# Performance work log

Measured on AMD Instinct MI355X. Metric: run time of the kernel, lower is better.

## Reference

```python
import jax, jax.numpy as jnp
import numpy as np

S0 = 100.0
V0 = 0.04
RATE = 0.025
MC = 50000          # MC_samples; 2*MC antithetic paths
N_STEPS = 180       # == int(x[:,0].max()), pinned in setup_inputs for static shapes
WIDTH = 64
N_OPTS = 32
H = 1.0 / 360.0     # timegrid step: (maxT/360)/maxT


def setup_inputs():
    key = jax.random.key(0)
    ks = jax.random.split(key, 8)
    mat = jax.random.randint(ks[0], (N_OPTS,), 30, N_STEPS + 1).astype(jnp.float32)
    mat = mat.at[0].set(float(N_STEPS))  # pin max maturity -> static n_steps
    strikes = 80.0 + 40.0 * jax.random.uniform(ks[1], (N_OPTS,), dtype=jnp.float32)
    x = jnp.stack([mat, strikes], axis=1)  # [n_opts, 2]: (maturity_days, strike)
    z = jax.random.normal(ks[2], (MC, N_STEPS), dtype=jnp.float32)
    z1 = jax.random.normal(ks[3], (MC, N_STEPS), dtype=jnp.float32)
    # 4 stacked tiny MLPs: order = [driftS, diffusionS, driftV, diffusionV]
    W1 = 0.1 * jax.random.normal(ks[4], (4, WIDTH, 4), dtype=jnp.float32)
    b1 = jnp.zeros((4, WIDTH), jnp.float32)
    W2 = 0.1 * jax.random.normal(ks[5], (4, WIDTH, WIDTH), dtype=jnp.float32)
    b2 = jnp.zeros((4, WIDTH), jnp.float32)
    Wo = 0.05 * jax.random.normal(ks[6], (4, 1, WIDTH), dtype=jnp.float32)
    bo = jnp.zeros((4, 1), jnp.float32)
    return dict(x=x, z=z, z1=z1, W1=W1, b1=b1, W2=W2, b2=b2, Wo=Wo, bo=bo)


def _mlp4(inp, W1, b1, W2, b2, Wo, bo):
    # Evaluate the 4 tiny MLPs on the shared input [M,4] in one batched pass.
    h1 = jax.nn.relu(jnp.einsum('nwd,md->nmw', W1, inp) + b1[:, None, :])
    h2 = jax.nn.relu(jnp.einsum('nvw,nmw->nmv', W2, h1) + b2[:, None, :])
    out = jnp.einsum('now,nmw->nmo', Wo, h2) + bo[:, None, :]
    return out[..., 0]  # [4, M]


def _forward(x, z, z1, W1, b1, W2, b2, Wo, bo, remat=False):
    M = 2 * MC
    h = jnp.float32(H)
    sqh = jnp.sqrt(h)
    # correlated second Brownian: z1 <- -0.5*z + sqrt(0.75)*z1, then antithetic
    z1c = -0.5 * z + np.float32(np.sqrt(0.75)) * z1
    zf = jnp.concatenate([z, -z], axis=0)        # [M, T]
    z1f = jnp.concatenate([z1c, -z1c], axis=0)   # [M, T]
    tgrid = jnp.arange(N_STEPS, dtype=jnp.float32) * h  # t_{i-1}
    rate_col = jnp.full((M,), RATE, jnp.float32)

    def step(carry, xs):
        S, V = carry
        zc, z1cc, tc = xs
        dW = sqh * zc
        dW1 = sqh * z1cc
        inp = jnp.stack([jnp.full((M,), tc), S, V, rate_col], axis=1)  # [M,4]
        o = _mlp4(inp, W1, b1, W2, b2, Wo, bo)  # [4, M]
        Sn = jnp.maximum(S + o[0] * h + o[1] * dW, 0.0)   # max(., 0) clamp
        Vn = jnp.maximum(V + o[2] * h + o[3] * dW1, 0.0)
        return (Sn, Vn), Sn

    if remat:
        step = jax.checkpoint(step)
    init = (jnp.full((M,), S0, jnp.float32), jnp.full((M,), V0, jnp.float32))
    _, Spath = jax.lax.scan(step, init, (zf.T, z1f.T, tgrid))  # Spath: [T, M]
    Sample_path = jnp.concatenate([jnp.full((1, M), S0, jnp.float32), Spath], axis=0)  # [T+1, M]

    # vectorized option pricing over all rows of x
    idx = x[:, 0].astype(jnp.int32)                  # maturity index into path
    ST = Sample_path[idx]                            # [n_opts, M]
    payoff = jnp.maximum(ST - x[:, 1][:, None], 0.0)
    price = payoff.mean(axis=1) * jnp.exp(-RATE * x[:, 0] / 360.0)
    return price.reshape(-1, 1)


def reference(x, z, z1, W1, b1, W2, b2, Wo, bo):
    return _forward(x, z, z1, W1, b1, W2, b2, Wo, bo, remat=False)
```

## Files before the change

kernel.cpp:

```cpp
#include <hip/hip_runtime.h>
#include <math.h>

#define MC      50000
#define MPATHS  100000
#define NSTEPS  180
#define NOPTS   32

typedef __attribute__((ext_vector_type(8))) short short8;
typedef __attribute__((ext_vector_type(4))) float float4v;
typedef _Float16 half2v __attribute__((ext_vector_type(2)));
typedef unsigned u32x32 __attribute__((ext_vector_type(32)));

static __device__ __forceinline__ unsigned bf16u(float x) {
    unsigned u = __float_as_uint(x);
    return (u + 0x7fffu + ((u >> 16) & 1u)) >> 16;
}
static __device__ __forceinline__ float bf16val(float x) {
    return __uint_as_float(bf16u(x) << 16);
}
static __device__ __forceinline__ unsigned pkh2(float a, float b) {
    half2v h; h.x = (_Float16)a; h.y = (_Float16)b;
    return __builtin_bit_cast(unsigned, h);
}
static __device__ __forceinline__ unsigned pkrtz(float a, float b) {
    auto h = __builtin_amdgcn_cvt_pkrtz(a, b);
    return __builtin_bit_cast(unsigned, h);
}
static __device__ __forceinline__ float fdot2(unsigned w, unsigned h, float c) {
    return __builtin_amdgcn_fdot2(__builtin_bit_cast(half2v, w),
                                  __builtin_bit_cast(half2v, h), c, false);
}
static __device__ __forceinline__ short8 fr4(unsigned a, unsigned b,
                                             unsigned c, unsigned d) {
    union { unsigned u[4]; short8 s; } t;
    t.u[0] = a; t.u[1] = b; t.u[2] = c; t.u[3] = d;
    return t.s;
}
static __device__ __forceinline__ float4v mfma16(short8 a, short8 b, float4v c) {
    return __builtin_amdgcn_mfma_f32_16x16x32_bf16(a, b, c, 0, 0, 0);
}


__global__ void probe_mn(int* tbl) {
    const int lane = threadIdx.x;
    for (int s = lane; s < 2048; s += 64) tbl[s] = 0;
    const float4v z4 = {0.f, 0.f, 0.f, 0.f};
    for (int L = 0; L < 64; ++L)
        for (int j = 0; j < 8; ++j) {
            unsigned au[4] = {0u, 0u, 0u, 0u};
            if (lane == L) au[j >> 1] = 0x3F80u << (16 * (j & 1));
            short8 a = fr4(au[0], au[1], au[2], au[3]);
            short8 b = fr4(0x3F803F80u, 0x3F803F80u, 0x3F803F80u, 0x3F803F80u);
            float4v d = mfma16(a, b, z4);
            if ((lane & 15) == 0) {
                #pragma unroll
                for (int r = 0; r < 4; ++r)
                    if (d[r] != 0.0f) tbl[L * 8 + j] = (lane >> 4) * 4 + r;
            }
        }
    for (int L = 0; L < 64; ++L)
        for (int j = 0; j < 8; ++j) {
            unsigned bu[4] = {0u, 0u, 0u, 0u};
            if (lane == L) bu[j >> 1] = 0x3F80u << (16 * (j & 1));
            short8 a = fr4(0x3F803F80u, 0x3F803F80u, 0x3F803F80u, 0x3F803F80u);
            short8 b = fr4(bu[0], bu[1], bu[2], bu[3]);
            float4v d = mfma16(a, b, z4);
            if ((lane >> 4) == 0 && d[0] != 0.0f) tbl[1024 + L * 8 + j] = (lane & 15);
        }
}

__global__ void probe_k(int* tbl) {
    const int lane = threadIdx.x;
    const int sA = blockIdx.x;
    const float4v z4 = {0.f, 0.f, 0.f, 0.f};
    unsigned au[4] = {0u, 0u, 0u, 0u};
    if (lane == (sA >> 3)) au[(sA & 7) >> 1] = 0x3F80u << (16 * (sA & 1));
    short8 a = fr4(au[0], au[1], au[2], au[3]);
    int kid = -1;
    for (int sB = 0; sB < 512; ++sB) {
        unsigned bu[4] = {0u, 0u, 0u, 0u};
        const int LB = sB >> 3, jB = sB & 7;
        if (lane == LB) bu[jB >> 1] = 0x3F80u << (16 * (jB & 1));
        short8 b = fr4(bu[0], bu[1], bu[2], bu[3]);
        float4v d = mfma16(a, b, z4);
        bool hit = (d[0] != 0.f) | (d[1] != 0.f) | (d[2] != 0.f) | (d[3] != 0.f);
        if (__any(hit)) {
            if (kid < 0) kid = sB;
            if (lane == 0) tbl[1536 + sB] = kid;
        }
    }
    if (lane == 0) tbl[512 + sA] = (kid < 0) ? 0 : kid;
}

__global__ void finalize_verify(int* tbl, int* flag) {
    __shared__ int cnt[32];
    __shared__ int minv[32];
    const int lane = threadIdx.x;
    if (lane < 32) { cnt[lane] = 0; minv[lane] = 0; }
    int rA[8], rB[8];
    #pragma unroll
    for (int j = 0; j < 8; ++j) {
        const int s = lane * 8 + j;
        const int kidA = tbl[512 + s], kidB = tbl[1536 + s];
        int ra = 0, rb = 0;
        for (int u = 0; u < 512; ++u) {
            const int canon = (tbl[1536 + u] == u);
            ra += canon & (u < kidA);
            rb += canon & (u < kidB);
        }
        rA[j] = ra & 31; rB[j] = rb & 31;
    }
    __syncthreads();
    #pragma unroll
    for (int j = 0; j < 8; ++j) {
        tbl[512 + lane * 8 + j]  = rA[j];
        tbl[1536 + lane * 8 + j] = rB[j];
    }
    unsigned au[4] = {0u, 0u, 0u, 0u}, bu[4] = {0u, 0u, 0u, 0u};
    #pragma unroll
    for (int j = 0; j < 8; ++j) {
        const int s = lane * 8 + j;
        const int m = tbl[s] & 15, ka = rA[j];
        const int n = tbl[1024 + s] & 15, kb = rB[j];
        const int fv = ((m * 7 + ka * 3) % 5) - 2;
        const int gv = ((kb * 5 + n * 11) % 7) - 3;
        au[j >> 1] |= bf16u((float)fv) << (16 * (j & 1));
        bu[j >> 1] |= bf16u((float)gv) << (16 * (j & 1));
    }
    const float4v z4 = {0.f, 0.f, 0.f, 0.f};
    float4v d = mfma16(fr4(au[0], au[1], au[2], au[3]),
                       fr4(bu[0], bu[1], bu[2], bu[3]), z4);
    const int col = lane & 15;
    bool ok = true;
    #pragma unroll
    for (int r = 0; r < 4; ++r) {
        const int row = (lane >> 4) * 4 + r;
        int ref = 0;
        for (int k = 0; k < 32; ++k)
            ref += (((row * 7 + k * 3) % 5) - 2) * (((k * 5 + col * 11) % 7) - 3);
        ok = ok && (d[r] == (float)ref);
    }
    bool okf = ok;
    #pragma unroll
    for (int j = 0; j < 8; ++j) {
        okf = okf && ((tbl[1024 + lane * 8 + j] & 15) == (lane & 15));
        const int ref = __shfl(rB[j], lane & 48, 64);
        okf = okf && (rB[j] == ref);
    }
    if ((lane & 15) == 0) {
        const int g = lane >> 4;
        #pragma unroll
        for (int j = 0; j < 8; ++j) {
            atomicAdd(&cnt[rB[j]], 1);
            minv[rB[j]] = 16 * ((j >> 2) & 1) + 4 * g + 2 * ((j >> 1) & 1) + (j & 1);
        }
    }
    __syncthreads();
    if (lane < 32) {
        okf = okf && (cnt[lane] == 1);
        tbl[2048 + lane] = minv[lane];
    }
    const bool allok = __all(okf);
    if (lane == 0) *flag = allok ? 1 : 0;
}

__global__ void build_frags(const float* __restrict__ W1, const float* __restrict__ b1,
                            const float* __restrict__ W2, const int* __restrict__ tbl,
                            uint4* __restrict__ w1f, uint4* __restrict__ w2f) {
    const int t = blockIdx.x * 256 + threadIdx.x;
    if (t >= 3072) return;
    const int lane = t & 63, frag = t >> 6;
    const float rateB = bf16val(0.025f);
    unsigned u[4] = {0u, 0u, 0u, 0u};
    if (frag < 16) {
        const int net = frag >> 2, mt = frag & 3;
        #pragma unroll
        for (int j = 0; j < 8; ++j) {
            const int s = lane * 8 + j;
            const int m = tbl[s] & 15, k = tbl[512 + s] & 31;
            unsigned bits = 0u;
            if (k < 12) {
                const int kk = (k < 6) ? k : k - 6;
                const int M = net * 64 + 16 * mt + m;
                float v;
                if (kk == 0)                 v = W1[M * 4 + 0];
                else if (kk == 1 || kk == 4) v = W1[M * 4 + 1];
                else if (kk == 2 || kk == 5) v = W1[M * 4 + 2];
                else                         v = W1[M * 4 + 3] + b1[M] / rateB;
                bits = (k < 6) ? bf16u(v) : bf16u(v - bf16val(v));
            }
            u[j >> 1] |= bits << (16 * (j & 1));
        }
        w1f[frag * 64 + lane] = make_uint4(u[0], u[1], u[2], u[3]);
    } else {
        const int f2 = frag - 16;
        const int net = f2 >> 3, mt = (f2 >> 1) & 3, kc = f2 & 1;
        #pragma unroll
        for (int j = 0; j < 8; ++j) {
            const int s = lane * 8 + j;
            const int m = tbl[s] & 15, k = tbl[512 + s] & 31;
            const float v = W2[(net * 64 + 16 * mt + m) * 64 + 32 * kc + tbl[2048 + k]];
            u[j >> 1] |= bf16u(v) << (16 * (j & 1));
        }
        w2f[f2 * 64 + lane] = make_uint4(u[0], u[1], u[2], u[3]);
    }
}

__global__ __launch_bounds__(256, 3)
void sde_mfma_w4(const float* __restrict__ x, const float* __restrict__ z,
                 const float* __restrict__ z1, const float* __restrict__ b2,
                 const float* __restrict__ Wo, const float* __restrict__ bo,
                 const int* __restrict__ tbl, const uint4* __restrict__ w1f,
                 const uint4* __restrict__ w2f, const int* __restrict__ flag,
                 float* __restrict__ acc)
{
    if (*flag != 1) return;
    __shared__ __align__(16) float wo_s[256];
    __shared__ __align__(16) float b2_s[256];
    __shared__ float dxch[2][4][64];
    __shared__ float ls_k[NOPTS];
    __shared__ int   maskTab[NSTEPS + 4];

    const int tid = threadIdx.x;
    const int wv = tid >> 6, lane = tid & 63;
    const int q = lane >> 4, c = lane & 15;

    for (int j = tid; j < 256; j += 256) { wo_s[j] = Wo[j]; b2_s[j] = b2[j]; }
    for (int j = tid; j < NSTEPS + 4; j += 256) maskTab[j] = 0;
    if (tid < NOPTS) ls_k[tid] = x[2 * tid + 1];
    __syncthreads();
    if (tid < NOPTS) atomicOr(&maskTab[(int)x[2 * tid]], 1 << tid);
    __syncthreads();

    const unsigned rate16 = bf16u(0.025f);
    unsigned selAB[4], dynM[4], cU[4], mT[4];
    {
        int rowj[8];
        #pragma unroll
        for (int j = 0; j < 8; ++j) {
            const int kb = tbl[1536 + lane * 8 + j] & 31;
            rowj[j] = (kb < 6) ? kb : ((kb < 12) ? kb - 6 : 6);
        }
        #pragma unroll
        for (int w = 0; w < 4; ++w) {
            unsigned s = 0, d = 0, cu = 0, mt_ = 0;
            #pragma unroll
            for (int h = 0; h < 2; ++h) {
                const int r = rowj[2 * w + h];
                unsigned hs = 0x0504u, hd = 0u, hcu = 0u, hmt = 0u;
                if      (r == 1) { hs = 0x0504u; hd = 0xFFFFu; }
                else if (r == 2) { hs = 0x0706u; hd = 0xFFFFu; }
                else if (r == 4) { hs = 0x0100u; hd = 0xFFFFu; }
                else if (r == 5) { hs = 0x0302u; hd = 0xFFFFu; }
                else if (r == 0) { hmt = 0xFFFFu; }
                else if (r == 3) { hcu = rate16; }
                s  |= hs  << (16 * h); d   |= hd  << (16 * h);
                cu |= hcu << (16 * h); mt_ |= hmt << (16 * h);
            }
            selAB[w] = s; dynM[w] = d; cU[w] = cu; mT[w] = mt_;
        }
    }

    const int p_ = blockIdx.x * 64 + lane;
    const float wgt = (p_ < MPATHS) ? 1.0f : 0.0f;
    int pc = (p_ < MPATHS) ? p_ : (MPATHS - 1);
    float sgn = 1.0f; int row_ = pc;
    if (pc >= MC) { sgn = -1.0f; row_ -= MC; }
    const float* __restrict__ zrow  = z  + (size_t)row_ * NSTEPS;
    const float* __restrict__ z1row = z1 + (size_t)row_ * NSTEPS;

    const float hh = 1.0f / 360.0f, sqh = sqrtf(hh);
    const float s75 = 0.86602540378443864676f;
    const float bon = bo[wv];

    uint4 a1f[4], a2f[8];
    #pragma unroll
    for (int mt = 0; mt < 4; ++mt) {
        a1f[mt]         = w1f[(wv * 4 + mt) * 64 + lane];
        a2f[2 * mt]     = w2f[((wv * 4 + mt) * 2 + 0) * 64 + lane];
        a2f[2 * mt + 1] = w2f[((wv * 4 + mt) * 2 + 1) * 64 + lane];
    }

    float S = 100.0f, V = 0.04f;

    #pragma unroll 1
    for (int i = 0; i < NSTEPS; ++i) {
        float mult;
        if      (wv == 1) mult = sqh * (sgn * zrow[i]);
        else if (wv == 3) mult = sqh * (sgn * (-0.5f * zrow[i] + s75 * z1row[i]));
        else              mult = hh;

        const float t = (float)i * hh;
        const unsigned tB = bf16u(t);
        const unsigned tB2 = tB | (tB << 16);
        unsigned UW[4];
        #pragma unroll
        for (int w = 0; w < 4; ++w) UW[w] = cU[w] | (mT[w] & tB2);

        const unsigned Shu = bf16u(S), Vhu = bf16u(V);
        const unsigned PA = Shu | (Vhu << 16);
        const float Sr = S - __uint_as_float(Shu << 16);
        const float Vr = V - __uint_as_float(Vhu << 16);
        const unsigned PB = __builtin_amdgcn_perm(__float_as_uint(Vr),
                                                  __float_as_uint(Sr), 0x07060302u);

        unsigned B1[4][4];
        #pragma unroll
        for (int nt = 0; nt < 4; ++nt) {
            const int a = (nt << 6) | (c << 2);
            const unsigned Ap = (unsigned)__builtin_amdgcn_ds_bpermute(a, (int)PA);
            const unsigned Bp = (unsigned)__builtin_amdgcn_ds_bpermute(a, (int)PB);
            #pragma unroll
            for (int w = 0; w < 4; ++w)
                B1[nt][w] = (__builtin_amdgcn_perm(Ap, Bp, selAB[w]) & dynM[w]) | UW[w];
        }

        float part[4] = {0.f, 0.f, 0.f, 0.f};
        const float4v z4 = {0.f, 0.f, 0.f, 0.f};
        #pragma unroll
        for (int nt = 0; nt < 4; ++nt) {
            unsigned pk0[4], pk1[4];
            #pragma unroll
            for (int mt = 0; mt < 4; ++mt) {
                float4v d = mfma16(fr4(a1f[mt].x, a1f[mt].y, a1f[mt].z, a1f[mt].w),
                                   fr4(B1[nt][0], B1[nt][1], B1[nt][2], B1[nt][3]), z4);
                const unsigned r0 = __float_as_uint(fmaxf(d[0], 0.f));
                const unsigned r1 = __float_as_uint(fmaxf(d[1], 0.f));
                const unsigned r2 = __float_as_uint(fmaxf(d[2], 0.f));
                const unsigned r3 = __float_as_uint(fmaxf(d[3], 0.f));
                pk0[mt] = __builtin_amdgcn_perm(r1, r0, 0x07060302u);
                pk1[mt] = __builtin_amdgcn_perm(r3, r2, 0x07060302u);
            }
            const short8 Bk0 = fr4(pk0[0], pk1[0], pk0[1], pk1[1]);
            const short8 Bk1 = fr4(pk0[2], pk1[2], pk0[3], pk1[3]);
            #pragma unroll
            for (int mt = 0; mt < 4; ++mt) {
                const float4  wo4 = *(const float4*)&wo_s[wv * 64 + 16 * mt + 4 * q];
                const float4v c4  = *(const float4v*)&b2_s[wv * 64 + 16 * mt + 4 * q];
                float4v d = mfma16(fr4(a2f[2 * mt].x, a2f[2 * mt].y,
                                       a2f[2 * mt].z, a2f[2 * mt].w), Bk0, c4);
                d = mfma16(fr4(a2f[2 * mt + 1].x, a2f[2 * mt + 1].y,
                               a2f[2 * mt + 1].z, a2f[2 * mt + 1].w), Bk1, d);
                part[nt] += wo4.x * fmaxf(d[0], 0.f)
                          + wo4.y * fmaxf(d[1], 0.f)
                          + wo4.z * fmaxf(d[2], 0.f)
                          + wo4.w * fmaxf(d[3], 0.f);
            }
        }
        #pragma unroll
        for (int nt = 0; nt < 4; ++nt) {
            float s2 = part[nt];
            s2 += __shfl_xor(s2, 16, 64);
            s2 += __shfl_xor(s2, 32, 64);
            part[nt] = s2;
        }
        float o = (q == 0) ? part[0] : (q == 1) ? part[1] : (q == 2) ? part[2] : part[3];
        o += bon;

        dxch[i & 1][wv][lane] = o * mult;
        __syncthreads();
        const float dS = dxch[i & 1][0][lane] + dxch[i & 1][1][lane];
        const float dV = dxch[i & 1][2][lane] + dxch[i & 1][3][lane];
        S = fmaxf(S + dS, 0.0f);
        V = fmaxf(V + dV, 0.0f);

        if (wv == 0) {
            int mm = maskTab[i + 1];
            while (mm) {
                const int qq = __ffs(mm) - 1; mm &= mm - 1;
                float pay = wgt * fmaxf(S - ls_k[qq], 0.0f);
                #pragma unroll
                for (int off = 32; off > 0; off >>= 1)
                    pay += __shfl_down(pay, off, 64);
                if (lane == 0) atomicAdd(&acc[qq], pay);
            }
        }
    }
}

__global__ void pack_w(const float* __restrict__ W1, const float* __restrict__ W2,
                       unsigned* __restrict__ wp1, unsigned* __restrict__ wp2) {
    int i = blockIdx.x * 256 + threadIdx.x;
    if (i < 512)              wp1[i] = pkh2(W1[2 * i], W1[2 * i + 1]);
    else if (i < 512 + 8192) { int k = i - 512; wp2[k] = pkh2(W2[2 * k], W2[2 * k + 1]); }
}

__global__ __launch_bounds__(64, 2)
void sde_dot2(const float* __restrict__ x, const float* __restrict__ z,
              const float* __restrict__ z1, const float* __restrict__ b1,
              const float* __restrict__ b2, const float* __restrict__ Wo,
              const float* __restrict__ bo, const uint4* __restrict__ wp1,
              const uint4* __restrict__ wp2, const int* __restrict__ flag,
              float* __restrict__ acc)
{
    if (*flag == 1) return;
    __shared__ __align__(16) uint4 wlds[2176];
    __shared__ float ls_k[NOPTS];
    __shared__ int   maskTab[NSTEPS + 4];
    const int tid = threadIdx.x;
    for (int j = tid; j < 2176; j += 64) wlds[j] = (j < 128) ? wp1[j] : wp2[j - 128];
    for (int jj = tid; jj < NSTEPS + 4; jj += 64) maskTab[jj] = 0;
    if (tid < NOPTS) ls_k[tid] = x[2 * tid + 1];
    __syncthreads();
    if (tid < NOPTS) atomicOr(&maskTab[(int)x[2 * tid]], 1 << tid);
    __syncthreads();
    const int pA = blockIdx.x * 128 + tid, pB = pA + 64;
    const float wgtA = (pA < MPATHS) ? 1.0f : 0.0f;
    const float wgtB = (pB < MPATHS) ? 1.0f : 0.0f;
    int pcA = (pA < MPATHS) ? pA : (MPATHS - 1);
    int pcB = (pB < MPATHS) ? pB : (MPATHS - 1);
    float sgnA = 1.0f, sgnB = 1.0f; int rowA = pcA, rowB = pcB;
    if (pcA >= MC) { sgnA = -1.0f; rowA -= MC; }
    if (pcB >= MC) { sgnB = -1.0f; rowB -= MC; }
    const float* __restrict__ zA  = z  + (size_t)rowA * NSTEPS;
    const float* __restrict__ z1A = z1 + (size_t)rowA * NSTEPS;
    const float* __restrict__ zB  = z  + (size_t)rowB * NSTEPS;
    const float* __restrict__ z1B = z1 + (size_t)rowB * NSTEPS;
    const float hh = 1.0f / 360.0f, sqh = sqrtf(hh);
    const float s75 = 0.86602540378443864676f, rate = 0.025f;
    float SA = 100.0f, VA = 0.04f, SB = 100.0f, VB = 0.04f;
    #pragma unroll 1
    for (int i = 0; i < NSTEPS; ++i) {
        const float zcrA = zA[i], z1rA = z1A[i], zcrB = zB[i], z1rB = z1B[i];
        const float dWA = sqh * (sgnA * zcrA);
        const float dW1A = sqh * (sgnA * (-0.5f * zcrA + s75 * z1rA));
        const float dWB = sqh * (sgnB * zcrB);
        const float dW1B = sqh * (sgnB * (-0.5f * zcrB + s75 * z1rB));
        const float t = (float)i * hh;
        const unsigned inA01 = pkrtz(t, SA), inA23 = pkrtz(VA, rate);
        const unsigned inB01 = pkrtz(t, SB), inB23 = pkrtz(VB, rate);
        float dSA = 0.f, dVA = 0.f, dSB = 0.f, dVB = 0.f;
        #pragma unroll 1
        for (int net = 0; net < 4; ++net) {
            const float* __restrict__ b1n = b1 + net * 64;
            const float* __restrict__ b2n = b2 + net * 64;
            const float* __restrict__ won = Wo + net * 64;
            const uint4* __restrict__ wl1 = &wlds[net * 32];
            const uint4* __restrict__ wl2 = &wlds[128 + net * 512];
            u32x32 hA, hB;
            #pragma unroll
            for (int u = 0; u < 64; u += 2) {
                const uint4 wv = wl1[u >> 1];
                const float bb0 = b1n[u], bb1 = b1n[u + 1];
                float a0 = fdot2(wv.x, inA01, bb0); a0 = fdot2(wv.y, inA23, a0);
                float a1 = fdot2(wv.z, inA01, bb1); a1 = fdot2(wv.w, inA23, a1);
                float c0 = fdot2(wv.x, inB01, bb0); c0 = fdot2(wv.y, inB23, c0);
                float c1 = fdot2(wv.z, inB01, bb1); c1 = fdot2(wv.w, inB23, c1);
                hA[u >> 1] = pkrtz(fmaxf(a0, 0.f), fmaxf(a1, 0.f));
                hB[u >> 1] = pkrtz(fmaxf(c0, 0.f), fmaxf(c1, 0.f));
            }
            float outA = bo[net], outB = outA;
            #pragma unroll 1
            for (int j = 0; j < 64; j += 4) {
                const uint4* __restrict__ r0 = wl2 + (j + 0) * 8;
                const uint4* __restrict__ r1 = wl2 + (j + 1) * 8;
                const uint4* __restrict__ r2 = wl2 + (j + 2) * 8;
                const uint4* __restrict__ r3 = wl2 + (j + 3) * 8;
                float a0 = b2n[j], a1 = b2n[j + 1], a2 = b2n[j + 2], a3 = b2n[j + 3];
                float c0 = a0, c1 = a1, c2 = a2, c3 = a3;
                #pragma unroll
                for (int kk = 0; kk < 8; ++kk) {
                    const uint4 w0 = r0[kk], w1 = r1[kk], w2 = r2[kk], w3 = r3[kk];
                    const unsigned hA0 = hA[4 * kk], hA1 = hA[4 * kk + 1];
                    const unsigned hA2 = hA[4 * kk + 2], hA3 = hA[4 * kk + 3];
                    const unsigned hB0 = hB[4 * kk], hB1 = hB[4 * kk + 1];
                    const unsigned hB2 = hB[4 * kk + 2], hB3 = hB[4 * kk + 3];
                    a0 = fdot2(w0.x, hA0, a0); a0 = fdot2(w0.y, hA1, a0);
                    a0 = fdot2(w0.z, hA2, a0); a0 = fdot2(w0.w, hA3, a0);
                    a1 = fdot2(w1.x, hA0, a1); a1 = fdot2(w1.y, hA1, a1);
                    a1 = fdot2(w1.z, hA2, a1); a1 = fdot2(w1.w, hA3, a1);
                    a2 = fdot2(w2.x, hA0, a2); a2 = fdot2(w2.y, hA1, a2);
                    a2 = fdot2(w2.z, hA2, a2); a2 = fdot2(w2.w, hA3, a2);
                    a3 = fdot2(w3.x, hA0, a3); a3 = fdot2(w3.y, hA1, a3);
                    a3 = fdot2(w3.z, hA2, a3); a3 = fdot2(w3.w, hA3, a3);
                    c0 = fdot2(w0.x, hB0, c0); c0 = fdot2(w0.y, hB1, c0);
                    c0 = fdot2(w0.z, hB2, c0); c0 = fdot2(w0.w, hB3, c0);
                    c1 = fdot2(w1.x, hB0, c1); c1 = fdot2(w1.y, hB1, c1);
                    c1 = fdot2(w1.z, hB2, c1); c1 = fdot2(w1.w, hB3, c1);
                    c2 = fdot2(w2.x, hB0, c2); c2 = fdot2(w2.y, hB1, c2);
                    c2 = fdot2(w2.z, hB2, c2); c2 = fdot2(w2.w, hB3, c2);
                    c3 = fdot2(w3.x, hB0, c3); c3 = fdot2(w3.y, hB1, c3);
                    c3 = fdot2(w3.z, hB2, c3); c3 = fdot2(w3.w, hB3, c3);
                }
                const float wo0 = won[j], wo1 = won[j + 1];
                const float wo2 = won[j + 2], wo3 = won[j + 3];
                outA = fmaf(wo0, fmaxf(a0, 0.f), outA); outA = fmaf(wo1, fmaxf(a1, 0.f), outA);
                outA = fmaf(wo2, fmaxf(a2, 0.f), outA); outA = fmaf(wo3, fmaxf(a3, 0.f), outA);
                outB = fmaf(wo0, fmaxf(c0, 0.f), outB); outB = fmaf(wo1, fmaxf(c1, 0.f), outB);
                outB = fmaf(wo2, fmaxf(c2, 0.f), outB); outB = fmaf(wo3, fmaxf(c3, 0.f), outB);
            }
            const float msA = (net == 0) ? hh : (net == 1) ? dWA  : 0.0f;
            const float mvA = (net == 2) ? hh : (net == 3) ? dW1A : 0.0f;
            const float msB = (net == 0) ? hh : (net == 1) ? dWB  : 0.0f;
            const float mvB = (net == 2) ? hh : (net == 3) ? dW1B : 0.0f;
            dSA = fmaf(outA, msA, dSA); dVA = fmaf(outA, mvA, dVA);
            dSB = fmaf(outB, msB, dSB); dVB = fmaf(outB, mvB, dVB);
        }
        SA = fmaxf(SA + dSA, 0.f); VA = fmaxf(VA + dVA, 0.f);
        SB = fmaxf(SB + dSB, 0.f); VB = fmaxf(VB + dVB, 0.f);
        int mm = maskTab[i + 1];
        while (mm) {
            const int qq = __ffs(mm) - 1; mm &= mm - 1;
            float pay = wgtA * fmaxf(SA - ls_k[qq], 0.f) + wgtB * fmaxf(SB - ls_k[qq], 0.f);
            #pragma unroll
            for (int off = 32; off > 0; off >>= 1)
                pay += __shfl_down(pay, off, 64);
            if (tid == 0) atomicAdd(&acc[qq], pay);
        }
    }
}

__global__ void price_kernel(const float* __restrict__ x, const float* __restrict__ acc,
                             float* __restrict__ out) {
    const int q = threadIdx.x;
    if (q < NOPTS) {
        const float mat = x[q * 2];
        out[q] = acc[q] * (1.0f / (float)MPATHS) * expf((-0.025f * mat) / 360.0f);
    }
}

extern "C" void kernel_launch(void* const* d_in, const int* in_sizes, int n_in,
                              void* d_out, int out_size, void* d_ws, size_t ws_size,
                              hipStream_t stream)
{
    const float* x  = (const float*)d_in[0];
    const float* z  = (const float*)d_in[1];
    const float* z1 = (const float*)d_in[2];
    const float* W1 = (const float*)d_in[3];
    const float* b1 = (const float*)d_in[4];
    const float* W2 = (const float*)d_in[5];
    const float* b2 = (const float*)d_in[6];
    const float* Wo = (const float*)d_in[7];
    const float* bo = (const float*)d_in[8];

    char* ws = (char*)d_ws;
    float*    acc  = (float*)ws;
    int*      flag = (int*)(ws + 256);
    int*      tbl  = (int*)(ws + 1024);
    uint4*    w1f  = (uint4*)(ws + 16384);
    uint4*    w2f  = (uint4*)(ws + 32768);
    unsigned* wp1  = (unsigned*)(ws + 65536);
    unsigned* wp2  = wp1 + 512;

    (void)hipMemsetAsync(acc, 0, NOPTS * sizeof(float), stream);
    pack_w<<<(512 + 8192 + 255) / 256, 256, 0, stream>>>(W1, W2, wp1, wp2);
    probe_mn<<<1, 64, 0, stream>>>(tbl);
    probe_k<<<512, 64, 0, stream>>>(tbl);
    finalize_verify<<<1, 64, 0, stream>>>(tbl, flag);
    build_frags<<<12, 256, 0, stream>>>(W1, b1, W2, tbl, w1f, w2f);

    const int gridS = (MPATHS + 63) / 64;
    sde_mfma_w4<<<gridS, 256, 0, stream>>>(x, z, z1, b2, Wo, bo, tbl, w1f, w2f, flag, acc);
    const int gridF = (MPATHS + 127) / 128;
    sde_dot2<<<gridF, 64, 0, stream>>>(x, z, z1, b1, b2, Wo, bo,
                                       (const uint4*)wp1, (const uint4*)wp2, flag, acc);
    price_kernel<<<1, 64, 0, stream>>>(x, acc, (float*)d_out);
}
```

Baseline: 1.608 ms.

## Process two 64-path groups per block to amortize weights and barriers

Each block of the MFMA SDE kernel now advances 128 paths (two independent 64-lane groups A and B) instead of 64, interleaving their MFMA chains and halving the grid. This amortizes the per-block weight-fragment loads, the shared-memory exchange and the per-step __syncthreads over twice the work, and gives the scheduler two independent MFMA dependency chains to hide latency. In exchange, register pressure roughly doubles for the per-step intermediates, which could reduce occupancy under launch_bounds(256,3) or cause spills, and there are fewer blocks to spread across CUs.

```diff
diff --git a/kernel.cpp b/kernel.cpp
--- a/kernel.cpp
+++ b/kernel.cpp
@@ -217,7 +217,7 @@
     if (*flag != 1) return;
     __shared__ __align__(16) float wo_s[256];
     __shared__ __align__(16) float b2_s[256];
-    __shared__ float dxch[2][4][64];
+    __shared__ float dxch[2][4][128];
     __shared__ float ls_k[NOPTS];
     __shared__ int   maskTab[NSTEPS + 4];
 
@@ -261,13 +261,19 @@
         }
     }
 
-    const int p_ = blockIdx.x * 64 + lane;
-    const float wgt = (p_ < MPATHS) ? 1.0f : 0.0f;
-    int pc = (p_ < MPATHS) ? p_ : (MPATHS - 1);
-    float sgn = 1.0f; int row_ = pc;
-    if (pc >= MC) { sgn = -1.0f; row_ -= MC; }
-    const float* __restrict__ zrow  = z  + (size_t)row_ * NSTEPS;
-    const float* __restrict__ z1row = z1 + (size_t)row_ * NSTEPS;
+    const int pA_ = blockIdx.x * 128 + lane;
+    const int pB_ = pA_ + 64;
+    const float wgtA = (pA_ < MPATHS) ? 1.0f : 0.0f;
+    const float wgtB = (pB_ < MPATHS) ? 1.0f : 0.0f;
+    int pcA = (pA_ < MPATHS) ? pA_ : (MPATHS - 1);
+    int pcB = (pB_ < MPATHS) ? pB_ : (MPATHS - 1);
+    float sgnA = 1.0f, sgnB = 1.0f; int rwA = pcA, rwB = pcB;
+    if (pcA >= MC) { sgnA = -1.0f; rwA -= MC; }
+    if (pcB >= MC) { sgnB = -1.0f; rwB -= MC; }
+    const float* __restrict__ zrA  = z  + (size_t)rwA * NSTEPS;
+    const float* __restrict__ z1rA = z1 + (size_t)rwA * NSTEPS;
+    const float* __restrict__ zrB  = z  + (size_t)rwB * NSTEPS;
+    const float* __restrict__ z1rB = z1 + (size_t)rwB * NSTEPS;
 
     const float hh = 1.0f / 360.0f, sqh = sqrtf(hh);
     const float s75 = 0.86602540378443864676f;
@@ -281,14 +287,20 @@
         a2f[2 * mt + 1] = w2f[((wv * 4 + mt) * 2 + 1) * 64 + lane];
     }
 
-    float S = 100.0f, V = 0.04f;
+    float SA = 100.0f, VA = 0.04f, SB = 100.0f, VB = 0.04f;
 
     #pragma unroll 1
     for (int i = 0; i < NSTEPS; ++i) {
-        float mult;
-        if      (wv == 1) mult = sqh * (sgn * zrow[i]);
-        else if (wv == 3) mult = sqh * (sgn * (-0.5f * zrow[i] + s75 * z1row[i]));
-        else              mult = hh;
+        float multA, multB;
+        if (wv == 1) {
+            multA = sqh * (sgnA * zrA[i]);
+            multB = sqh * (sgnB * zrB[i]);
+        } else if (wv == 3) {
+            multA = sqh * (sgnA * (-0.5f * zrA[i] + s75 * z1rA[i]));
+            multB = sqh * (sgnB * (-0.5f * zrB[i] + s75 * z1rB[i]));
+        } else {
+            multA = hh; multB = hh;
+        }
 
         const float t = (float)i * hh;
         const unsigned tB = bf16u(t);
@@ -297,78 +309,113 @@
         #pragma unroll
         for (int w = 0; w < 4; ++w) UW[w] = cU[w] | (mT[w] & tB2);
 
-        const unsigned Shu = bf16u(S), Vhu = bf16u(V);
-        const unsigned PA = Shu | (Vhu << 16);
-        const float Sr = S - __uint_as_float(Shu << 16);
-        const float Vr = V - __uint_as_float(Vhu << 16);
-        const unsigned PB = __builtin_amdgcn_perm(__float_as_uint(Vr),
-                                                  __float_as_uint(Sr), 0x07060302u);
-
-        unsigned B1[4][4];
+        const unsigned ShuA = bf16u(SA), VhuA = bf16u(VA);
+        const unsigned PAA = ShuA | (VhuA << 16);
+        const float SrA = SA - __uint_as_float(ShuA << 16);
+        const float VrA = VA - __uint_as_float(VhuA << 16);
+        const unsigned PBA = __builtin_amdgcn_perm(__float_as_uint(VrA),
+                                                   __float_as_uint(SrA), 0x07060302u);
+        const unsigned ShuB = bf16u(SB), VhuB = bf16u(VB);
+        const unsigned PAB = ShuB | (VhuB << 16);
+        const float SrB = SB - __uint_as_float(ShuB << 16);
+        const float VrB = VB - __uint_as_float(VhuB << 16);
+        const unsigned PBB = __builtin_amdgcn_perm(__float_as_uint(VrB),
+                                                   __float_as_uint(SrB), 0x07060302u);
+
+        float part[2][4] = {{0.f, 0.f, 0.f, 0.f}, {0.f, 0.f, 0.f, 0.f}};
+        const float4v z4 = {0.f, 0.f, 0.f, 0.f};
+
         #pragma unroll
         for (int nt = 0; nt < 4; ++nt) {
             const int a = (nt << 6) | (c << 2);
-            const unsigned Ap = (unsigned)__builtin_amdgcn_ds_bpermute(a, (int)PA);
-            const unsigned Bp = (unsigned)__builtin_amdgcn_ds_bpermute(a, (int)PB);
+            const unsigned ApA = (unsigned)__builtin_amdgcn_ds_bpermute(a, (int)PAA);
+            const unsigned BpA = (unsigned)__builtin_amdgcn_ds_bpermute(a, (int)PBA);
+            const unsigned ApB = (unsigned)__builtin_amdgcn_ds_bpermute(a, (int)PAB);
+            const unsigned BpB = (unsigned)__builtin_amdgcn_ds_bpermute(a, (int)PBB);
+            unsigned B1A[4], B1B[4];
             #pragma unroll
-            for (int w = 0; w < 4; ++w)
-                B1[nt][w] = (__builtin_amdgcn_perm(Ap, Bp, selAB[w]) & dynM[w]) | UW[w];
-        }
-
-        float part[4] = {0.f, 0.f, 0.f, 0.f};
-        const float4v z4 = {0.f, 0.f, 0.f, 0.f};
-        #pragma unroll
-        for (int nt = 0; nt < 4; ++nt) {
-            unsigned pk0[4], pk1[4];
+            for (int w = 0; w < 4; ++w) {
+                B1A[w] = (__builtin_amdgcn_perm(ApA, BpA, selAB[w]) & dynM[w]) | UW[w];
+                B1B[w] = (__builtin_amdgcn_perm(ApB, BpB, selAB[w]) & dynM[w]) | UW[w];
+            }
+            unsigned pkA0[4], pkA1[4], pkB0[4], pkB1[4];
             #pragma unroll
             for (int mt = 0; mt < 4; ++mt) {
-                float4v d = mfma16(fr4(a1f[mt].x, a1f[mt].y, a1f[mt].z, a1f[mt].w),
-                                   fr4(B1[nt][0], B1[nt][1], B1[nt][2], B1[nt][3]), z4);
-                const unsigned r0 = __float_as_uint(fmaxf(d[0], 0.f));
-                const unsigned r1 = __float_as_uint(fmaxf(d[1], 0.f));
-                const unsigned r2 = __float_as_uint(fmaxf(d[2], 0.f));
-                const unsigned r3 = __float_as_uint(fmaxf(d[3], 0.f));
-                pk0[mt] = __builtin_amdgcn_perm(r1, r0, 0x07060302u);
-                pk1[mt] = __builtin_amdgcn_perm(r3, r2, 0x07060302u);
-            }
-            const short8 Bk0 = fr4(pk0[0], pk1[0], pk0[1], pk1[1]);
-            const short8 Bk1 = fr4(pk0[2], pk1[2], pk0[3], pk1[3]);
+                const short8 A1 = fr4(a1f[mt].x, a1f[mt].y, a1f[mt].z, a1f[mt].w);
+                float4v dA = mfma16(A1, fr4(B1A[0], B1A[1], B1A[2], B1A[3]), z4);
+                float4v dB = mfma16(A1, fr4(B1B[0], B1B[1], B1B[2], B1B[3]), z4);
+                const unsigned a0 = __float_as_uint(fmaxf(dA[0], 0.f));
+                const unsigned a1 = __float_as_uint(fmaxf(dA[1], 0.f));
+                const unsigned a2 = __float_as_uint(fmaxf(dA[2], 0.f));
+                const unsigned a3 = __float_as_uint(fmaxf(dA[3], 0.f));
+                pkA0[mt] = __builtin_amdgcn_perm(a1, a0, 0x07060302u);
+                pkA1[mt] = __builtin_amdgcn_perm(a3, a2, 0x07060302u);
+                const unsigned b0 = __float_as_uint(fmaxf(dB[0], 0.f));
+                const unsigned b1_ = __float_as_uint(fmaxf(dB[1], 0.f));
+                const unsigned b2_ = __float_as_uint(fmaxf(dB[2], 0.f));
+                const unsigned b3 = __float_as_uint(fmaxf(dB[3], 0.f));
+                pkB0[mt] = __builtin_amdgcn_perm(b1_, b0, 0x07060302u);
+                pkB1[mt] = __builtin_amdgcn_perm(b3, b2_, 0x07060302u);
+            }
+            const short8 BkA0 = fr4(pkA0[0], pkA1[0], pkA0[1], pkA1[1]);
+            const short8 BkA1 = fr4(pkA0[2], pkA1[2], pkA0[3], pkA1[3]);
+            const short8 BkB0 = fr4(pkB0[0], pkB1[0], pkB0[1], pkB1[1]);
+            const short8 BkB1 = fr4(pkB0[2], pkB1[2], pkB0[3], pkB1[3]);
             #pragma unroll
             for (int mt = 0; mt < 4; ++mt) {
                 const float4  wo4 = *(const float4*)&wo_s[wv * 64 + 16 * mt + 4 * q];
                 const float4v c4  = *(const float4v*)&b2_s[wv * 64 + 16 * mt + 4 * q];
-                float4v d = mfma16(fr4(a2f[2 * mt].x, a2f[2 * mt].y,
-                                       a2f[2 * mt].z, a2f[2 * mt].w), Bk0, c4);
-                d = mfma16(fr4(a2f[2 * mt + 1].x, a2f[2 * mt + 1].y,
-                               a2f[2 * mt + 1].z, a2f[2 * mt + 1].w), Bk1, d);
-                part[nt] += wo4.x * fmaxf(d[0], 0.f)
-                          + wo4.y * fmaxf(d[1], 0.f)
-                          + wo4.z * fmaxf(d[2], 0.f)
-                          + wo4.w * fmaxf(d[3], 0.f);
-            }
-        }
-        #pragma unroll
-        for (int nt = 0; nt < 4; ++nt) {
-            float s2 = part[nt];
-            s2 += __shfl_xor(s2, 16, 64);
-            s2 += __shfl_xor(s2, 32, 64);
-            part[nt] = s2;
-        }
-        float o = (q == 0) ? part[0] : (q == 1) ? part[1] : (q == 2) ? part[2] : part[3];
-        o += bon;
-
-        dxch[i & 1][wv][lane] = o * mult;
+                const short8 A20 = fr4(a2f[2 * mt].x, a2f[2 * mt].y,
+                                       a2f[2 * mt].z, a2f[2 * mt].w);
+                const short8 A21 = fr4(a2f[2 * mt + 1].x, a2f[2 * mt + 1].y,
+                                       a2f[2 * mt + 1].z, a2f[2 * mt + 1].w);
+                float4v dA = mfma16(A20, BkA0, c4);
+                dA = mfma16(A21, BkA1, dA);
+                float4v dB = mfma16(A20, BkB0, c4);
+                dB = mfma16(A21, BkB1, dB);
+                part[0][nt] += wo4.x * fmaxf(dA[0], 0.f)
+                             + wo4.y * fmaxf(dA[1], 0.f)
+                             + wo4.z * fmaxf(dA[2], 0.f)
+                             + wo4.w * fmaxf(dA[3], 0.f);
+                part[1][nt] += wo4.x * fmaxf(dB[0], 0.f)
+                             + wo4.y * fmaxf(dB[1], 0.f)
+                             + wo4.z * fmaxf(dB[2], 0.f)
+                             + wo4.w * fmaxf(dB[3], 0.f);
+            }
+        }
+        #pragma unroll
+        for (int g = 0; g < 2; ++g)
+            #pragma unroll
+            for (int nt = 0; nt < 4; ++nt) {
+                float s2 = part[g][nt];
+                s2 += __shfl_xor(s2, 16, 64);
+                s2 += __shfl_xor(s2, 32, 64);
+                part[g][nt] = s2;
+            }
+        float oA = (q == 0) ? part[0][0] : (q == 1) ? part[0][1]
+                 : (q == 2) ? part[0][2] : part[0][3];
+        float oB = (q == 0) ? part[1][0] : (q == 1) ? part[1][1]
+                 : (q == 2) ? part[1][2] : part[1][3];
+        oA += bon; oB += bon;
+
+        dxch[i & 1][wv][lane]      = oA * multA;
+        dxch[i & 1][wv][64 + lane] = oB * multB;
         __syncthreads();
-        const float dS = dxch[i & 1][0][lane] + dxch[i & 1][1][lane];
-        const float dV = dxch[i & 1][2][lane] + dxch[i & 1][3][lane];
-        S = fmaxf(S + dS, 0.0f);
-        V = fmaxf(V + dV, 0.0f);
+        const float dSA = dxch[i & 1][0][lane]      + dxch[i & 1][1][lane];
+        const float dVA = dxch[i & 1][2][lane]      + dxch[i & 1][3][lane];
+        const float dSB = dxch[i & 1][0][64 + lane] + dxch[i & 1][1][64 + lane];
+        const float dVB = dxch[i & 1][2][64 + lane] + dxch[i & 1][3][64 + lane];
+        SA = fmaxf(SA + dSA, 0.0f);
+        VA = fmaxf(VA + dVA, 0.0f);
+        SB = fmaxf(SB + dSB, 0.0f);
+        VB = fmaxf(VB + dVB, 0.0f);
 
         if (wv == 0) {
             int mm = maskTab[i + 1];
             while (mm) {
                 const int qq = __ffs(mm) - 1; mm &= mm - 1;
-                float pay = wgt * fmaxf(S - ls_k[qq], 0.0f);
+                float pay = wgtA * fmaxf(SA - ls_k[qq], 0.0f)
+                          + wgtB * fmaxf(SB - ls_k[qq], 0.0f);
                 #pragma unroll
                 for (int off = 32; off > 0; off >>= 1)
                     pay += __shfl_down(pay, off, 64);
@@ -549,7 +596,7 @@
     finalize_verify<<<1, 64, 0, stream>>>(tbl, flag);
     build_frags<<<12, 256, 0, stream>>>(W1, b1, W2, tbl, w1f, w2f);
 
-    const int gridS = (MPATHS + 63) / 64;
+    const int gridS = (MPATHS + 127) / 128;
     sde_mfma_w4<<<gridS, 256, 0, stream>>>(x, z, z1, b2, Wo, bo, tbl, w1f, w2f, flag, acc);
     const int gridF = (MPATHS + 127) / 128;
     sde_dot2<<<gridF, 64, 0, stream>>>(x, z, z1, b1, b2, Wo, bo,
```

Result: slower. 1.722 ms (+7.1%).
